# Performance work log

Measured on AMD Instinct MI355X. Metric: run time of the kernel, lower is better.

## Reference

```python
import jax, jax.numpy as jnp
import numpy as np

B, N, H, HID, LOCALITY = 2, 4096, 4, 256, 30.0
VD = HID // H
F32_MAX = jnp.finfo(jnp.float32).max


def setup_inputs() -> dict:
    key = jax.random.key(0)
    k1, k2, k3, k4 = jax.random.split(key, 4)
    m_dist = jax.random.uniform(k1, (B, N, N), dtype=jnp.float32)  # pairwise distances (b,N,N)
    x = jax.random.normal(k2, (B, N, HID), dtype=jnp.float32)
    r = jax.random.normal(k3, (1, H, 1, 1), dtype=jnp.float32)  # learned per-head distance scale
    # lecun_normal: std = 1/sqrt(fan_in), fan_in = HID
    weight = jax.random.normal(k4, (H, HID, VD), dtype=jnp.float32) / np.sqrt(HID)
    return {"m_dist": m_dist, "x": x, "r": r, "weight": weight}


def reference(m_dist, x, r, weight):
    # scaled distance per head: (b,h,n,n)
    scaled = m_dist[:, None, :, :] * (r ** 2)
    # percentile-thresholded local mask (linear interpolation, per row)
    thresh = jnp.percentile(scaled, LOCALITY, axis=-1, keepdims=True, method="linear")
    scaled = jnp.where(scaled <= thresh, scaled, F32_MAX)
    att = jax.nn.softmax(-scaled, axis=-1)  # (b,h,n,n)
    value = jnp.einsum("bnj,hjk->bhnk", x, weight)  # (b,h,n,v)
    out = jnp.einsum("bhnj,bhjd->bhnd", att, value)  # (b,h,n,v)
    out = jnp.transpose(out, (0, 2, 1, 3)).reshape(out.shape[0], -1, HID)  # (b,n,hid)
    return jax.nn.gelu(out, approximate=False)
```

## Files before the change

### kernel.cpp

```cpp
#include <hip/hip_runtime.h>
#include <hip/hip_bf16.h>

#define Bc   2
#define Nc   4096
#define Hc   4
#define HIDc 256
#define VDc  64

typedef short s8v  __attribute__((ext_vector_type(8)));
typedef float f4v  __attribute__((ext_vector_type(4)));

#define XSP 260

__global__ __launch_bounds__(256) void value_kernel(
    const float* __restrict__ x, const float* __restrict__ wgt,
    unsigned short* __restrict__ vt_g)
{
    __shared__ float xs[64 * XSP];
    __shared__ unsigned short ob[64 * 64];

    int t  = threadIdx.x;
    int bid = blockIdx.x;
    int nt = bid & 63;
    int h  = (bid >> 6) & 3;
    int b  = bid >> 8;
    int n0 = nt * 64;

    const float* xg = x + ((size_t)b * Nc + n0) * HIDc;
    #pragma unroll
    for (int i = 0; i < 16; i++) {
        int id = t + i * 256;
        int row = id >> 6, ch = id & 63;
        *(float4*)&xs[row * XSP + ch * 4] = ((const float4*)xg)[id];
    }
    __syncthreads();

    int k4 = t & 15;
    int ns = t >> 4;
    const float4* wg4 = (const float4*)(wgt + (size_t)h * HIDc * VDc);

    float4 acc[4];
    #pragma unroll
    for (int i = 0; i < 4; i++) acc[i] = (float4){0.f, 0.f, 0.f, 0.f};

    for (int j = 0; j < HIDc; j += 4) {
        float4 w0 = wg4[(j + 0) * 16 + k4];
        float4 w1 = wg4[(j + 1) * 16 + k4];
        float4 w2 = wg4[(j + 2) * 16 + k4];
        float4 w3 = wg4[(j + 3) * 16 + k4];
        #pragma unroll
        for (int i = 0; i < 4; i++) {
            float4 xv = *(const float4*)&xs[(ns + i * 16) * XSP + j];
            acc[i].x += xv.x * w0.x + xv.y * w1.x + xv.z * w2.x + xv.w * w3.x;
            acc[i].y += xv.x * w0.y + xv.y * w1.y + xv.z * w2.y + xv.w * w3.y;
            acc[i].z += xv.x * w0.z + xv.y * w1.z + xv.z * w2.z + xv.w * w3.z;
            acc[i].w += xv.x * w0.w + xv.y * w1.w + xv.z * w2.w + xv.w * w3.w;
        }
    }
    #pragma unroll
    for (int i = 0; i < 4; i++) {
        int nn = ns + i * 16;
        float a[4] = {acc[i].x, acc[i].y, acc[i].z, acc[i].w};
        #pragma unroll
        for (int c = 0; c < 4; c++) {
            __hip_bfloat16 hb = __float2bfloat16(a[c]);
            ob[(k4 * 4 + c) * 64 + nn] = *(unsigned short*)&hb;
        }
    }
    __syncthreads();

    unsigned short* vg = vt_g + (((size_t)b * Hc + h) * VDc) * Nc + n0;
    #pragma unroll
    for (int i = 0; i < 16; i++) {
        int idx = t + i * 256;
        int kk = idx >> 6, nn = idx & 63;
        vg[(size_t)kk * Nc + nn] = ob[idx];
    }
}

__global__ __launch_bounds__(256) void thresh_kernel(
    const float* __restrict__ m_dist,
    float* __restrict__ thr_out, float* __restrict__ min_out)
{
    __shared__ unsigned int hist[1024];
    __shared__ float wred[4];
    __shared__ unsigned int wscan[4];
    __shared__ int b0s, b1s;
    __shared__ unsigned int c0s;
    __shared__ unsigned int ncand;
    __shared__ float cand[256];
    __shared__ float s0s, s1s;

    int t = threadIdx.x;
    size_t rowid = blockIdx.x;
    const float* row = m_dist + rowid * Nc;

    for (int i = t; i < 1024; i += 256) hist[i] = 0u;
    if (t == 0) ncand = 0u;
    __syncthreads();

    float4 vals[4];
    float lmin = 1e30f;
    #pragma unroll
    for (int i = 0; i < 4; i++) {
        float4 v = ((const float4*)row)[t + i * 256];
        vals[i] = v;
        lmin = fminf(lmin, fminf(fminf(v.x, v.y), fminf(v.z, v.w)));
        atomicAdd(&hist[min(1023, (int)(v.x * 1024.0f))], 1u);
        atomicAdd(&hist[min(1023, (int)(v.y * 1024.0f))], 1u);
        atomicAdd(&hist[min(1023, (int)(v.z * 1024.0f))], 1u);
        atomicAdd(&hist[min(1023, (int)(v.w * 1024.0f))], 1u);
    }
    #pragma unroll
    for (int o = 32; o > 0; o >>= 1) lmin = fminf(lmin, __shfl_xor(lmin, o));
    if ((t & 63) == 0) wred[t >> 6] = lmin;
    __syncthreads();
    float rmin = fminf(fminf(wred[0], wred[1]), fminf(wred[2], wred[3]));

    unsigned int c[4], csum = 0;
    #pragma unroll
    for (int j = 0; j < 4; j++) { c[j] = hist[t * 4 + j]; csum += c[j]; }
    unsigned int inc = csum;
    #pragma unroll
    for (int o = 1; o < 64; o <<= 1) {
        unsigned int nv = __shfl_up(inc, o);
        if ((t & 63) >= o) inc += nv;
    }
    if ((t & 63) == 63) wscan[t >> 6] = inc;
    __syncthreads();
    unsigned int wpref = 0;
    for (int wv = 0; wv < (t >> 6); wv++) wpref += wscan[wv];
    unsigned int P = wpref + inc - csum;

    const unsigned int R0 = 1228u, R1 = 1229u;
    unsigned int cum = P;
    #pragma unroll
    for (int j = 0; j < 4; j++) {
        unsigned int lo = cum, hi = cum + c[j];
        if (R0 >= lo && R0 < hi) { b0s = t * 4 + j; c0s = lo; }
        if (R1 >= lo && R1 < hi) { b1s = t * 4 + j; }
        cum = hi;
    }
    __syncthreads();
    int b0 = b0s, b1 = b1s;
    unsigned int C0 = c0s;

    #pragma unroll
    for (int i = 0; i < 4; i++) {
        float a[4] = {vals[i].x, vals[i].y, vals[i].z, vals[i].w};
        #pragma unroll
        for (int j = 0; j < 4; j++) {
            int bx = min(1023, (int)(a[j] * 1024.0f));
            if (bx >= b0 && bx <= b1) {
                unsigned int p = atomicAdd(&ncand, 1u);
                if (p < 256u) cand[p] = a[j];
            }
        }
    }
    __syncthreads();
    unsigned int nc = min(ncand, 256u);
    if ((unsigned int)t < nc) {
        float v = cand[t];
        unsigned int rk = C0;
        for (unsigned int j = 0; j < nc; j++) {
            float u = cand[j];
            rk += (u < v || (u == v && j < (unsigned int)t)) ? 1u : 0u;
        }
        if (rk == R0) s0s = v;
        if (rk == R1) s1s = v;
    }
    __syncthreads();
    if (t == 0) {
        thr_out[rowid] = 0.5f * (s0s + s1s);
        min_out[rowid] = rmin;
    }
}

#define NT 32
#define JT 64
#define BIGF 3.0e38f

__global__ __launch_bounds__(512, 8) void attn_kernel(
    const float* __restrict__ m_dist, const float* __restrict__ rr,
    const unsigned short* __restrict__ vt_g,
    const float* __restrict__ thr_g, const float* __restrict__ min_g,
    float* __restrict__ Op, float* __restrict__ Zp, int jlen)
{
    __shared__ float ms[NT * 64];
    __shared__ unsigned short vt[Hc * VDc * 64];

    int t = threadIdx.x;
    const int nblk = Bc * (Nc / NT);
    int js = blockIdx.x / nblk;
    int rb = blockIdx.x - js * nblk;
    int b  = rb >> 7;
    int n0 = (rb & 127) * NT;
    int j0 = js * jlen;

    int lane = t & 63, q = lane >> 4, m16 = lane & 15;
    int w = t >> 6;
    int h = w & 3, rh = w >> 2;
    int row = rh * 16 + m16;

    float mn = min_g[b * Nc + n0 + row];
    float rv = rr[h];
    float cc = -(rv * rv) * 1.4426950408889634f;
    float nmncc = -mn * cc;

    f4v acc[4];
    #pragma unroll
    for (int ct = 0; ct < 4; ct++) acc[ct] = (f4v){0.f, 0.f, 0.f, 0.f};
    float zacc = 0.f;

    const float* mbase = m_dist + ((size_t)b * Nc + n0) * Nc + j0;
    const unsigned short* vtb = vt_g + ((size_t)b * Hc * VDc) * Nc + j0;

    int mrow = t >> 4, mch = t & 15;
    int msw  = mrow * 64 + ((mch ^ (mrow & 15)) << 2);
    float thm = thr_g[b * Nc + n0 + mrow];
    int vrow0 = t >> 3, vch = t & 7;

    int a00 = row * 64 + (((q * 2 + 0) ^ m16) << 2);
    int a01 = row * 64 + (((q * 2 + 1) ^ m16) << 2);
    int a10 = row * 64 + (((8 + q * 2 + 0) ^ m16) << 2);
    int a11 = row * 64 + (((8 + q * 2 + 1) ^ m16) << 2);

    for (int jt = 0; jt < jlen; jt += JT) {
        {
            float4 v = *(const float4*)(mbase + (size_t)mrow * Nc + jt + mch * 4);
            v.x = (v.x <= thm) ? v.x : BIGF;
            v.y = (v.y <= thm) ? v.y : BIGF;
            v.z = (v.z <= thm) ? v.z : BIGF;
            v.w = (v.w <= thm) ? v.w : BIGF;
            *(float4*)&ms[msw] = v;
        }
        #pragma unroll
        for (int i = 0; i < 4; i++) {
            int rrow = vrow0 + i * 64;
            *(float4*)&vt[rrow * 64 + ((vch ^ (rrow & 7)) << 3)] =
                *(const float4*)(vtb + (size_t)rrow * Nc + jt + vch * 8);
        }
        __syncthreads();

        const unsigned short* vb = &vt[(h * VDc) * 64];
        #pragma unroll
        for (int ks = 0; ks < 2; ks++) {
            float4 a0 = *(const float4*)&ms[ks ? a10 : a00];
            float4 a1 = *(const float4*)&ms[ks ? a11 : a01];
            float w0 = __builtin_amdgcn_exp2f(__builtin_fmaf(a0.x, cc, nmncc));
            float w1 = __builtin_amdgcn_exp2f(__builtin_fmaf(a0.y, cc, nmncc));
            float w2 = __builtin_amdgcn_exp2f(__builtin_fmaf(a0.z, cc, nmncc));
            float w3 = __builtin_amdgcn_exp2f(__builtin_fmaf(a0.w, cc, nmncc));
            float w4 = __builtin_amdgcn_exp2f(__builtin_fmaf(a1.x, cc, nmncc));
            float w5 = __builtin_amdgcn_exp2f(__builtin_fmaf(a1.y, cc, nmncc));
            float w6 = __builtin_amdgcn_exp2f(__builtin_fmaf(a1.z, cc, nmncc));
            float w7 = __builtin_amdgcn_exp2f(__builtin_fmaf(a1.w, cc, nmncc));
            zacc += ((w0 + w1) + (w2 + w3)) + ((w4 + w5) + (w6 + w7));
            union { s8v v; __hip_bfloat162 h2[4]; } afu;
            afu.h2[0] = __float22bfloat162_rn((float2){w0, w1});
            afu.h2[1] = __float22bfloat162_rn((float2){w2, w3});
            afu.h2[2] = __float22bfloat162_rn((float2){w4, w5});
            afu.h2[3] = __float22bfloat162_rn((float2){w6, w7});
            #pragma unroll
            for (int ct = 0; ct < 4; ct++) {
                int brow = ct * 16 + m16;
                s8v bf = *(const s8v*)(vb + brow * 64 + (((ks * 4 + q) ^ (m16 & 7)) << 3));
                acc[ct] = __builtin_amdgcn_mfma_f32_16x16x32_bf16(afu.v, bf, acc[ct], 0, 0, 0);
            }
        }
        __syncthreads();
    }

    zacc += __shfl_xor(zacc, 16);
    zacc += __shfl_xor(zacc, 32);
    if (q == 0)
        Zp[(((size_t)js * Bc + b) * Hc + h) * Nc + n0 + row] = zacc;

    #pragma unroll
    for (int ct = 0; ct < 4; ct++) {
        #pragma unroll
        for (int rg = 0; rg < 4; rg++) {
            int nl = rh * 16 + q * 4 + rg;
            Op[(((size_t)js * Bc + b) * Nc + n0 + nl) * HIDc + h * VDc + ct * 16 + m16]
                = acc[ct][rg];
        }
    }
}

__global__ __launch_bounds__(256) void combine_kernel(
    const float* __restrict__ Op, const float* __restrict__ Zp,
    float* __restrict__ out, int S)
{
    int g = blockIdx.x * 256 + threadIdx.x;
    int c4 = g & 63;
    int n  = (g >> 6) & (Nc - 1);
    int b  = g >> 18;
    int h  = c4 >> 4;

    float z = 0.f;
    float4 v = {0.f, 0.f, 0.f, 0.f};
    for (int s = 0; s < S; s++) {
        z += Zp[(((size_t)s * Bc + b) * Hc + h) * Nc + n];
        float4 p = *(const float4*)&Op[(((size_t)s * Bc + b) * Nc + n) * HIDc + c4 * 4];
        v.x += p.x; v.y += p.y; v.z += p.z; v.w += p.w;
    }
    float iz = 1.0f / z;
    float4 o;
    float u;
    u = v.x * iz; o.x = 0.5f * u * (1.0f + erff(u * 0.7071067811865476f));
    u = v.y * iz; o.y = 0.5f * u * (1.0f + erff(u * 0.7071067811865476f));
    u = v.z * iz; o.z = 0.5f * u * (1.0f + erff(u * 0.7071067811865476f));
    u = v.w * iz; o.w = 0.5f * u * (1.0f + erff(u * 0.7071067811865476f));
    *(float4*)&out[(((size_t)b * Nc + n) * HIDc) + c4 * 4] = o;
}

extern "C" void kernel_launch(void* const* d_in, const int* in_sizes, int n_in,
                              void* d_out, int out_size, void* d_ws, size_t ws_size,
                              hipStream_t stream) {
    const float* m_dist = (const float*)d_in[0];
    const float* x      = (const float*)d_in[1];
    const float* r      = (const float*)d_in[2];
    const float* weight = (const float*)d_in[3];
    float* out = (float*)d_out;

    char* ws = (char*)d_ws;
    const size_t MB = 1024 * 1024;
    unsigned short* vt = (unsigned short*)ws;
    float* thr = (float*)(ws + 4 * MB);
    float* mn  = (float*)(ws + 4 * MB + 32 * 1024);
    float* Zp  = (float*)(ws + 4 * MB + 64 * 1024);
    float* Op  = (float*)(ws + 5 * MB);

    int S = 4;
    if (ws_size < 5 * MB + 4 * (size_t)(Bc * Nc * HIDc * 4)) S = 2;
    if (ws_size < 5 * MB + 2 * (size_t)(Bc * Nc * HIDc * 4)) S = 1;
    int jlen = Nc / S;

    value_kernel<<<512, 256, 0, stream>>>(x, weight, vt);
    thresh_kernel<<<Bc * Nc, 256, 0, stream>>>(m_dist, thr, mn);
    attn_kernel<<<S * Bc * (Nc / NT), 512, 0, stream>>>(m_dist, r, vt, thr, mn, Op, Zp, jlen);
    combine_kernel<<<(Bc * Nc * HIDc) / 1024, 256, 0, stream>>>(Op, Zp, out, S);
}
```

Measured before the change: 280.8 us.

## Refine percentile histogram to a narrow window and load V tiles directly into LDS

The threshold kernel now builds its 1024-bin histogram over a narrow value window around the expected 30th percentile. Values below the window are counted separately, and the kernel falls back to the full [0,1] range if the target ranks fall outside the window. The finer bins should yield fewer candidates for the exact rank-selection step. In the attention kernel, the bf16 value-tile staging switches from load-to-register-then-store-to-LDS to global_load_lds direct-to-LDS transfers, keeping the same XOR swizzle layout, to cut VGPR traffic and instruction count. The fallback loop adds a possible second histogram pass, and the direct loads depend on correct wait/sync handling before LDS reads.

```diff
diff --git a/kernel.cpp b/kernel.cpp
--- a/kernel.cpp
+++ b/kernel.cpp
@@ -83,7 +83,8 @@
     float* __restrict__ thr_out, float* __restrict__ min_out)
 {
     __shared__ unsigned int hist[1024];
-    __shared__ float wred[4];
+    __shared__ float wredf[4];
+    __shared__ unsigned int wsum[4];
     __shared__ unsigned int wscan[4];
     __shared__ int b0s, b1s;
     __shared__ unsigned int c0s;
@@ -95,10 +96,6 @@
     size_t rowid = blockIdx.x;
     const float* row = m_dist + rowid * Nc;
 
-    for (int i = t; i < 1024; i += 256) hist[i] = 0u;
-    if (t == 0) ncand = 0u;
-    __syncthreads();
-
     float4 vals[4];
     float lmin = 1e30f;
     #pragma unroll
@@ -106,54 +103,87 @@
         float4 v = ((const float4*)row)[t + i * 256];
         vals[i] = v;
         lmin = fminf(lmin, fminf(fminf(v.x, v.y), fminf(v.z, v.w)));
-        atomicAdd(&hist[min(1023, (int)(v.x * 1024.0f))], 1u);
-        atomicAdd(&hist[min(1023, (int)(v.y * 1024.0f))], 1u);
-        atomicAdd(&hist[min(1023, (int)(v.z * 1024.0f))], 1u);
-        atomicAdd(&hist[min(1023, (int)(v.w * 1024.0f))], 1u);
     }
     #pragma unroll
     for (int o = 32; o > 0; o >>= 1) lmin = fminf(lmin, __shfl_xor(lmin, o));
-    if ((t & 63) == 0) wred[t >> 6] = lmin;
-    __syncthreads();
-    float rmin = fminf(fminf(wred[0], wred[1]), fminf(wred[2], wred[3]));
-
-    unsigned int c[4], csum = 0;
-    #pragma unroll
-    for (int j = 0; j < 4; j++) { c[j] = hist[t * 4 + j]; csum += c[j]; }
-    unsigned int inc = csum;
-    #pragma unroll
-    for (int o = 1; o < 64; o <<= 1) {
-        unsigned int nv = __shfl_up(inc, o);
-        if ((t & 63) >= o) inc += nv;
-    }
-    if ((t & 63) == 63) wscan[t >> 6] = inc;
-    __syncthreads();
-    unsigned int wpref = 0;
-    for (int wv = 0; wv < (t >> 6); wv++) wpref += wscan[wv];
-    unsigned int P = wpref + inc - csum;
+    if ((t & 63) == 0) wredf[t >> 6] = lmin;
 
     const unsigned int R0 = 1228u, R1 = 1229u;
-    unsigned int cum = P;
-    #pragma unroll
-    for (int j = 0; j < 4; j++) {
-        unsigned int lo = cum, hi = cum + c[j];
-        if (R0 >= lo && R0 < hi) { b0s = t * 4 + j; c0s = lo; }
-        if (R1 >= lo && R1 < hi) { b1s = t * 4 + j; }
-        cum = hi;
-    }
-    __syncthreads();
-    int b0 = b0s, b1 = b1s;
-    unsigned int C0 = c0s;
-
+    float wlo = 0.25f, whi = 0.35f;
+    int b0 = 0, b1 = 0;
+    unsigned int C0 = 0;
+
+    for (;;) {
+        float wscale = 1024.0f / (whi - wlo);
+
+        for (int i = t; i < 1024; i += 256) hist[i] = 0u;
+        if (t == 0) ncand = 0u;
+        __syncthreads();
+
+        unsigned int cb = 0;
+        #pragma unroll
+        for (int i = 0; i < 4; i++) {
+            float a[4] = {vals[i].x, vals[i].y, vals[i].z, vals[i].w};
+            #pragma unroll
+            for (int j = 0; j < 4; j++) {
+                float v = a[j];
+                if (v < wlo) {
+                    cb++;
+                } else {
+                    int bx = (int)((v - wlo) * wscale);
+                    if (bx < 1024) atomicAdd(&hist[bx], 1u);
+                }
+            }
+        }
+        #pragma unroll
+        for (int o = 32; o > 0; o >>= 1) cb += __shfl_xor(cb, o);
+        if ((t & 63) == 0) wsum[t >> 6] = cb;
+        __syncthreads();
+        unsigned int Cb = wsum[0] + wsum[1] + wsum[2] + wsum[3];
+
+        unsigned int c[4], csum = 0;
+        #pragma unroll
+        for (int j = 0; j < 4; j++) { c[j] = hist[t * 4 + j]; csum += c[j]; }
+        unsigned int inc = csum;
+        #pragma unroll
+        for (int o = 1; o < 64; o <<= 1) {
+            unsigned int nv = __shfl_up(inc, o);
+            if ((t & 63) >= o) inc += nv;
+        }
+        if ((t & 63) == 63) wscan[t >> 6] = inc;
+        __syncthreads();
+        unsigned int wpref = 0;
+        for (int wv = 0; wv < (t >> 6); wv++) wpref += wscan[wv];
+        unsigned int T = wscan[0] + wscan[1] + wscan[2] + wscan[3];
+        unsigned int P = Cb + wpref + inc - csum;
+
+        unsigned int cum = P;
+        #pragma unroll
+        for (int j = 0; j < 4; j++) {
+            unsigned int lo = cum, hi = cum + c[j];
+            if (R0 >= lo && R0 < hi) { b0s = t * 4 + j; c0s = lo; }
+            if (R1 >= lo && R1 < hi) { b1s = t * 4 + j; }
+            cum = hi;
+        }
+        __syncthreads();
+
+        if (Cb <= R0 && R1 < Cb + T) { b0 = b0s; b1 = b1s; C0 = c0s; break; }
+        wlo = 0.0f; whi = 1.001f;
+    }
+
+    float wscale = 1024.0f / (whi - wlo);
     #pragma unroll
     for (int i = 0; i < 4; i++) {
         float a[4] = {vals[i].x, vals[i].y, vals[i].z, vals[i].w};
         #pragma unroll
         for (int j = 0; j < 4; j++) {
-            int bx = min(1023, (int)(a[j] * 1024.0f));
-            if (bx >= b0 && bx <= b1) {
-                unsigned int p = atomicAdd(&ncand, 1u);
-                if (p < 256u) cand[p] = a[j];
+            float v = a[j];
+            if (v >= wlo) {
+                int bx = (int)((v - wlo) * wscale);
+                if (bx >= b0 && bx <= b1) {
+                    unsigned int p = atomicAdd(&ncand, 1u);
+                    if (p < 256u) cand[p] = v;
+                }
             }
         }
     }
@@ -172,7 +202,7 @@
     __syncthreads();
     if (t == 0) {
         thr_out[rowid] = 0.5f * (s0s + s1s);
-        min_out[rowid] = rmin;
+        min_out[rowid] = fminf(fminf(wredf[0], wredf[1]), fminf(wredf[2], wredf[3]));
     }
 }
 
@@ -218,7 +248,10 @@
     int mrow = t >> 4, mch = t & 15;
     int msw  = mrow * 64 + ((mch ^ (mrow & 15)) << 2);
     float thm = thr_g[b * Nc + n0 + mrow];
-    int vrow0 = t >> 3, vch = t & 7;
+
+    int srowl   = lane >> 3;
+    int schunk8 = ((lane & 7) ^ srowl) * 8;
+    unsigned short* vt_wbase = &vt[(w * 8) * 64];
 
     int a00 = row * 64 + (((q * 2 + 0) ^ m16) << 2);
     int a01 = row * 64 + (((q * 2 + 1) ^ m16) << 2);
@@ -226,6 +259,16 @@
     int a11 = row * 64 + (((8 + q * 2 + 1) ^ m16) << 2);
 
     for (int jt = 0; jt < jlen; jt += JT) {
+        #pragma unroll
+        for (int i = 0; i < 4; i++) {
+            int rrow = w * 8 + srowl + i * 64;
+            __builtin_amdgcn_global_load_lds(
+                (const __attribute__((address_space(1))) void*)
+                    (vtb + (size_t)rrow * Nc + jt + schunk8),
+                (__attribute__((address_space(3))) void*)
+                    (vt_wbase + i * 64 * 64),
+                16, 0, 0);
+        }
         {
             float4 v = *(const float4*)(mbase + (size_t)mrow * Nc + jt + mch * 4);
             v.x = (v.x <= thm) ? v.x : BIGF;
@@ -233,12 +276,6 @@
             v.z = (v.z <= thm) ? v.z : BIGF;
             v.w = (v.w <= thm) ? v.w : BIGF;
             *(float4*)&ms[msw] = v;
-        }
-        #pragma unroll
-        for (int i = 0; i < 4; i++) {
-            int rrow = vrow0 + i * 64;
-            *(float4*)&vt[rrow * 64 + ((vch ^ (rrow & 7)) << 3)] =
-                *(const float4*)(vtb + (size_t)rrow * Nc + jt + vch * 8);
         }
         __syncthreads();
 
```

After: 275.5 us. No clear change (-1.9%).
